# Performance work log

Hardware: AMD Instinct MI355X
Metric: run time of the kernel (lower is better)

Reference implementation:

```python
import jax, jax.numpy as jnp
import numpy as np
import math

B, S, E = 2, 4096, 2048
H, HKV, DK, DV = 16, 4, 128, 128
WIN = 512
EPS = 1e-5
NEG = -1e30


def setup_inputs() -> dict:
    key = jax.random.key(0)
    ks = jax.random.split(key, 8)
    scale = 1.0 / math.sqrt(E)
    return {
        "embeddings": jax.random.normal(ks[0], (B, S, E), dtype=jnp.float32),
        "cos_buffer": jax.random.uniform(ks[1], (2, 1, S, DK), dtype=jnp.float32),
        "sin_buffer": jax.random.uniform(ks[2], (2, 1, S, DK), dtype=jnp.float32),
        "wq": jax.random.normal(ks[3], (E, H * DK), dtype=jnp.float32) * scale,
        "wk": jax.random.normal(ks[4], (E, HKV * DK), dtype=jnp.float32) * scale,
        "wv": jax.random.normal(ks[5], (E, HKV * DV), dtype=jnp.float32) * scale,
        "wo": jax.random.normal(ks[6], (H * DV, E), dtype=jnp.float32) * (1.0 / math.sqrt(H * DV)),
        "window_size": WIN,
    }


def _rotate(f, cos, sin):
    half = f.shape[-1] // 2
    swapped = jnp.concatenate([f[..., half:], f[..., :half]], axis=-1)
    return cos * f + sin * swapped


def reference(embeddings, cos_buffer, sin_buffer, wq, wk, wv, wo, window_size):
    b, s, _ = embeddings.shape
    normed = embeddings * jax.lax.rsqrt(
        jnp.mean(jnp.square(embeddings), axis=-1, keepdims=True) + EPS)
    q = (normed @ wq).reshape(b, s, H, DK).transpose(0, 2, 1, 3)
    k = (normed @ wk).reshape(b, s, HKV, DK).transpose(0, 2, 1, 3)
    v = (normed @ wv).reshape(b, s, HKV, DV).transpose(0, 2, 1, 3)

    q = _rotate(q, cos_buffer[0], sin_buffer[0])
    k = _rotate(k, cos_buffer[1], sin_buffer[1])

    g = H // HKV
    k = jnp.repeat(k, g, axis=1)
    v = jnp.repeat(v, g, axis=1)

    W = window_size
    nb = s // W
    qb = q.reshape(b, H, nb, W, DK)
    kb = k.reshape(b, H, nb, W, DK)
    vb = v.reshape(b, H, nb, W, DV)
    k_prev = jnp.pad(kb, ((0, 0), (0, 0), (1, 0), (0, 0), (0, 0)))[:, :, :nb]
    v_prev = jnp.pad(vb, ((0, 0), (0, 0), (1, 0), (0, 0), (0, 0)))[:, :, :nb]
    kcat = jnp.concatenate([k_prev, kb], axis=3)
    vcat = jnp.concatenate([v_prev, vb], axis=3)

    scores = jnp.einsum('bhnqd,bhnkd->bhnqk', qb, kcat) / math.sqrt(DK)

    i = jnp.arange(W)[:, None]
    j = jnp.arange(2 * W)[None, :]
    base = (j > i) & (j <= i + W)
    blk = jnp.arange(nb)[:, None, None]
    mask = base[None] & ((blk > 0) | (j[None] >= W))
    scores = jnp.where(mask[None, None], scores, NEG)

    probs = jax.nn.softmax(scores, axis=-1)
    out = jnp.einsum('bhnqk,bhnkd->bhnqd', probs, vcat)
    out = out.reshape(b, H, s, DV).transpose(0, 2, 1, 3).reshape(b, s, H * DV)
    out = out @ wo
    return embeddings + out
```

## Files before the change

### kernel.cpp

```cpp
#include <hip/hip_runtime.h>

typedef unsigned short u16;
typedef __attribute__((ext_vector_type(8))) short s16x8;
typedef __attribute__((ext_vector_type(8))) unsigned short u16x8;
typedef __attribute__((ext_vector_type(4))) unsigned short u16x4;
typedef __attribute__((ext_vector_type(4))) float f32x4;

#define DEV __device__ __forceinline__

DEV u16 f2bf(float x) {
  union { float f; unsigned u; } c; c.f = x;
  unsigned r = c.u + 0x7FFFu + ((c.u >> 16) & 1u);
  return (u16)(r >> 16);
}
DEV float bf2f(u16 u) {
  union { unsigned u; float f; } c; c.u = ((unsigned)u) << 16;
  return c.f;
}
DEV void gload_lds16(const void* g, void* l) {
  __builtin_amdgcn_global_load_lds((const __attribute__((address_space(1))) void*)g,
                                   (__attribute__((address_space(3))) void*)l, 16, 0, 0);
}

__global__ __launch_bounds__(256) void k_rmsnorm(const float* __restrict__ emb, u16* __restrict__ X) {
  const int row = blockIdx.x;
  const int t = threadIdx.x;
  const float4* p4 = (const float4*)(emb + (size_t)row * 2048);
  float4 v0 = p4[t * 2], v1 = p4[t * 2 + 1];
  float ss = v0.x * v0.x + v0.y * v0.y + v0.z * v0.z + v0.w * v0.w
           + v1.x * v1.x + v1.y * v1.y + v1.z * v1.z + v1.w * v1.w;
  for (int off = 32; off; off >>= 1) ss += __shfl_xor(ss, off);
  __shared__ float red[4];
  if ((t & 63) == 0) red[t >> 6] = ss;
  __syncthreads();
  float tot = red[0] + red[1] + red[2] + red[3];
  float inv = rsqrtf(tot * (1.0f / 2048.0f) + 1e-5f);
  float v[8] = {v0.x, v0.y, v0.z, v0.w, v1.x, v1.y, v1.z, v1.w};
  u16x8 o;
  for (int j = 0; j < 8; ++j) o[j] = f2bf(v[j] * inv);
  *(u16x8*)(X + (size_t)row * 2048 + t * 8) = o;
}

__global__ __launch_bounds__(256) void k_transpose(const float* __restrict__ src, u16* __restrict__ dst,
                                                   int C, int dstStride) {
  __shared__ float tile[32][33];
  const int bc = blockIdx.x * 32, br = blockIdx.y * 32;
  const int tx = threadIdx.x & 31, ty = threadIdx.x >> 5;
  for (int i = 0; i < 32; i += 8)
    tile[ty + i][tx] = src[(size_t)(br + ty + i) * C + bc + tx];
  __syncthreads();
  for (int i = 0; i < 32; i += 8)
    dst[(size_t)(bc + ty + i) * dstStride + br + tx] = f2bf(tile[tx][ty + i]);
}

template <int EPI>
__global__ __launch_bounds__(256) void k_gemm_bt(const u16* __restrict__ A, const u16* __restrict__ Bt,
                                                 const int N, const int K,
                                                 u16* __restrict__ Cb, const float* __restrict__ Emb,
                                                 float* __restrict__ Cf,
                                                 u16* __restrict__ VtOut, const int vcol0) {
  __shared__ u16 As[128 * 32], Bs[128 * 32];
  const int t = threadIdx.x, w = t >> 6, l = t & 63;
  const int g = l >> 4, cc = l & 15;
  const int wr = w >> 1, wc = w & 1;
  const size_t m0 = (size_t)blockIdx.y * 128, n0 = (size_t)blockIdx.x * 128;
  const int lrow = l >> 2, lcol = (l & 3) * 8;
  f32x4 acc[4][4];
  for (int mi = 0; mi < 4; ++mi)
    for (int ni = 0; ni < 4; ++ni) acc[mi][ni] = (f32x4){0.f, 0.f, 0.f, 0.f};
  for (int k0 = 0; k0 < K; k0 += 32) {
    __syncthreads();
    for (int i = 0; i < 2; ++i) {
      const int ca = w * 2 + i;
      gload_lds16(A + (m0 + ca * 16 + lrow) * K + k0 + lcol, As + ca * 512);
      gload_lds16(Bt + (n0 + ca * 16 + lrow) * K + k0 + lcol, Bs + ca * 512);
    }
    __syncthreads();
    s16x8 a[4], b[4];
    for (int mi = 0; mi < 4; ++mi) a[mi] = *(const s16x8*)&As[(wr * 64 + mi * 16 + cc) * 32 + g * 8];
    for (int ni = 0; ni < 4; ++ni) b[ni] = *(const s16x8*)&Bs[(wc * 64 + ni * 16 + cc) * 32 + g * 8];
    for (int mi = 0; mi < 4; ++mi)
      for (int ni = 0; ni < 4; ++ni)
        acc[mi][ni] = __builtin_amdgcn_mfma_f32_16x16x32_bf16(a[mi], b[ni], acc[mi][ni], 0, 0, 0);
  }
  if (EPI == 1) {
    for (int mi = 0; mi < 4; ++mi)
      for (int ni = 0; ni < 4; ++ni)
        for (int r = 0; r < 4; ++r) {
          const size_t row = m0 + wr * 64 + mi * 16 + g * 4 + r;
          const size_t col = n0 + wc * 64 + ni * 16 + cc;
          Cf[row * N + col] = acc[mi][ni][r] + Emb[row * N + col];
        }
  } else if ((int)n0 >= vcol0) {
    const int hkv = (int)(n0 - vcol0) >> 7;
    const int bb = (int)(m0 >> 12);
    const int s0base = (int)(m0 & 4095);
    u16* vdst = VtOut + (size_t)(bb * 4 + hkv) * 128 * 4096;
    for (int mi = 0; mi < 4; ++mi)
      for (int ni = 0; ni < 4; ++ni) {
        const int d = wc * 64 + ni * 16 + cc;
        const int s = s0base + wr * 64 + mi * 16 + g * 4;
        u16x4 o;
        for (int r = 0; r < 4; ++r) o[r] = f2bf(acc[mi][ni][r]);
        *(u16x4*)(vdst + (size_t)d * 4096 + s) = o;
      }
  } else {
    for (int mi = 0; mi < 4; ++mi)
      for (int ni = 0; ni < 4; ++ni)
        for (int r = 0; r < 4; ++r) {
          const size_t row = m0 + wr * 64 + mi * 16 + g * 4 + r;
          const size_t col = n0 + wc * 64 + ni * 16 + cc;
          Cb[row * N + col] = f2bf(acc[mi][ni][r]);
        }
  }
}

__global__ __launch_bounds__(192) void k_rope(const u16* __restrict__ qkv, const float* __restrict__ cosb,
                                              const float* __restrict__ sinb, u16* __restrict__ Q,
                                              u16* __restrict__ K) {
  const int row = blockIdx.x;
  const int b = row >> 12, s = row & 4095;
  const int t = threadIdx.x;
  const u16* src = qkv + (size_t)row * 3072;
  if (t < 128) {
    const int h = t >> 3, d0 = (t & 7) * 8;
    const float* cp = cosb + (size_t)s * 128;
    const float* sp = sinb + (size_t)s * 128;
    u16x8 lo = *(const u16x8*)(src + h * 128 + d0);
    u16x8 hi = *(const u16x8*)(src + h * 128 + d0 + 64);
    u16x8 olo, ohi;
    for (int j = 0; j < 8; ++j) {
      float fl = bf2f(lo[j]), fh = bf2f(hi[j]);
      olo[j] = f2bf(cp[d0 + j] * fl + sp[d0 + j] * fh);
      ohi[j] = f2bf(cp[d0 + 64 + j] * fh + sp[d0 + 64 + j] * fl);
    }
    u16* dq = Q + (((size_t)b * 16 + h) * 4096 + s) * 128;
    *(u16x8*)(dq + d0) = olo;
    *(u16x8*)(dq + d0 + 64) = ohi;
  } else if (t < 160) {
    const int idx = t - 128, hk = idx >> 3, d0 = (idx & 7) * 8;
    const float* cp = cosb + 524288 + (size_t)s * 128;
    const float* sp = sinb + 524288 + (size_t)s * 128;
    u16x8 lo = *(const u16x8*)(src + 2048 + hk * 128 + d0);
    u16x8 hi = *(const u16x8*)(src + 2048 + hk * 128 + d0 + 64);
    u16x8 olo, ohi;
    for (int j = 0; j < 8; ++j) {
      float fl = bf2f(lo[j]), fh = bf2f(hi[j]);
      olo[j] = f2bf(cp[d0 + j] * fl + sp[d0 + j] * fh);
      ohi[j] = f2bf(cp[d0 + 64 + j] * fh + sp[d0 + 64 + j] * fl);
    }
    u16* dk = K + (((size_t)b * 4 + hk) * 4096 + s) * 128;
    *(u16x8*)(dk + d0) = olo;
    *(u16x8*)(dk + d0 + 64) = ohi;
  }
}

__global__ __launch_bounds__(256) void k_attn(const u16* __restrict__ Q, const u16* __restrict__ K,
                                              const u16* __restrict__ Vt, u16* __restrict__ AO) {
  const int bid = blockIdx.x;
  const int lin = (bid & 7) * 128 + (bid >> 3);
  const int grp = lin >> 7;
  const int b = grp >> 2, hkv = grp & 3;
  const int rem = lin & 127;
  const int h = hkv * 4 + (rem >> 5);
  const int qt = rem & 31;

  const int t = threadIdx.x, w = t >> 6, l = t & 63, g = l >> 4, cc = l & 15;
  const int q0 = qt * 128;
  const u16* Qp = Q + (((size_t)b * 16 + h) * 4096 + q0) * 128;
  const u16* Kp = K + ((size_t)b * 4 + hkv) * 4096 * 128;
  const u16* Vp = Vt + ((size_t)b * 4 + hkv) * 128 * 4096;

  __shared__ u16 Kl[2][32 * 128];
  __shared__ u16 Vl[2][128 * 32];
  __shared__ u16 Ps[4][32 * 40];
  u16* myPs = &Ps[w][0];

  auto stage = [&](int kt, int bufi) {
    for (int pass = 0; pass < 2; ++pass) {
      const int m = pass * 256 + t;
      const int row = m >> 4, cst = m & 15;
      const int cor = cst ^ (row & 7);
      gload_lds16(Kp + (size_t)(kt * 32 + row) * 128 + cor * 8, &Kl[bufi][m * 8]);
    }
    for (int pass = 0; pass < 2; ++pass) {
      const int m = pass * 256 + t;
      const int d = m >> 2, cst = m & 3;
      const int cor = cst ^ (d & 3);
      gload_lds16(Vp + (size_t)d * 4096 + kt * 32 + cor * 8, &Vl[bufi][m * 8]);
    }
  };

  s16x8 qf[2][4];
  for (int mi = 0; mi < 2; ++mi)
    for (int kk = 0; kk < 4; ++kk)
      qf[mi][kk] = *(const s16x8*)(Qp + (size_t)(w * 32 + mi * 16 + cc) * 128 + kk * 32 + g * 8);

  f32x4 accO[2][8];
  for (int mi = 0; mi < 2; ++mi)
    for (int nd = 0; nd < 8; ++nd) accO[mi][nd] = (f32x4){0.f, 0.f, 0.f, 0.f};
  float mrun[2], lrun[2];
  for (int mi = 0; mi < 2; ++mi) { mrun[mi] = -1e30f; lrun[mi] = 0.f; }

  int lo = q0 - 511; if (lo < 0) lo = 0;
  const int kt_lo = lo >> 5, kt_hi = (q0 + 127) >> 5;
  const float scale = 0.08838834764831845f;

  int cur = 0;
  stage(kt_lo, 0);
  __syncthreads();

  for (int kt = kt_lo; kt <= kt_hi; ++kt) {
    if (kt < kt_hi) stage(kt + 1, cur ^ 1);

    f32x4 sc[2][2];
    for (int mi = 0; mi < 2; ++mi)
      for (int nk = 0; nk < 2; ++nk) sc[mi][nk] = (f32x4){0.f, 0.f, 0.f, 0.f};
    __builtin_amdgcn_s_setprio(1);
    for (int kk = 0; kk < 4; ++kk) {
      s16x8 kb[2];
      for (int nk = 0; nk < 2; ++nk) {
        const int row = nk * 16 + cc;
        kb[nk] = *(const s16x8*)&Kl[cur][row * 128 + (((kk * 4 + g) ^ (row & 7)) * 8)];
      }
      for (int mi = 0; mi < 2; ++mi)
        for (int nk = 0; nk < 2; ++nk)
          sc[mi][nk] = __builtin_amdgcn_mfma_f32_16x16x32_bf16(kb[nk], qf[mi][kk], sc[mi][nk], 0, 0, 0);
    }
    __builtin_amdgcn_s_setprio(0);

    const bool full = (kt * 32 >= q0 - 384) && (kt * 32 + 31 <= q0);

    for (int mi = 0; mi < 2; ++mi) {
      const int qpos = q0 + w * 32 + mi * 16 + cc;
      if (full) {
        for (int nk = 0; nk < 2; ++nk)
          for (int r = 0; r < 4; ++r) sc[mi][nk][r] *= scale;
      } else {
        for (int nk = 0; nk < 2; ++nk)
          for (int r = 0; r < 4; ++r) {
            const int kpos = kt * 32 + nk * 16 + g * 4 + r;
            const float v = sc[mi][nk][r] * scale;
            sc[mi][nk][r] = (kpos <= qpos && kpos + 512 > qpos) ? v : -1e30f;
          }
      }
      float rm = sc[mi][0][0];
      for (int nk = 0; nk < 2; ++nk)
        for (int r = 0; r < 4; ++r) rm = fmaxf(rm, sc[mi][nk][r]);
      rm = fmaxf(rm, __shfl_xor(rm, 16));
      rm = fmaxf(rm, __shfl_xor(rm, 32));
      const float mnew = fmaxf(mrun[mi], rm);
      float rs = 0.f;
      if (full) {
        for (int nk = 0; nk < 2; ++nk)
          for (int r = 0; r < 4; ++r) {
            float pv = __expf(sc[mi][nk][r] - mnew);
            sc[mi][nk][r] = pv;
            rs += pv;
          }
      } else {
        for (int nk = 0; nk < 2; ++nk)
          for (int r = 0; r < 4; ++r) {
            float pv = sc[mi][nk][r];
            pv = (pv <= -1e29f) ? 0.f : __expf(pv - mnew);
            sc[mi][nk][r] = pv;
            rs += pv;
          }
      }
      rs += __shfl_xor(rs, 16);
      rs += __shfl_xor(rs, 32);
      const float alpha = __expf(mrun[mi] - mnew);
      mrun[mi] = mnew;
      lrun[mi] = lrun[mi] * alpha + rs;
      for (int nd = 0; nd < 8; ++nd)
        for (int r = 0; r < 4; ++r) accO[mi][nd][r] *= alpha;
      for (int nk = 0; nk < 2; ++nk) {
        u16x4 o;
        for (int r = 0; r < 4; ++r) o[r] = f2bf(sc[mi][nk][r]);
        *(u16x4*)&myPs[(mi * 16 + cc) * 40 + nk * 16 + g * 4] = o;
      }
    }

    __builtin_amdgcn_s_setprio(1);
    {
      s16x8 pa[2];
      for (int mi = 0; mi < 2; ++mi)
        pa[mi] = *(const s16x8*)&myPs[(mi * 16 + cc) * 40 + g * 8];
      for (int nd = 0; nd < 8; ++nd) {
        const int d = nd * 16 + cc;
        s16x8 vb = *(const s16x8*)&Vl[cur][d * 32 + ((g ^ (d & 3)) * 8)];
        for (int mi = 0; mi < 2; ++mi)
          accO[mi][nd] = __builtin_amdgcn_mfma_f32_16x16x32_bf16(vb, pa[mi], accO[mi][nd], 0, 0, 0);
      }
    }
    __builtin_amdgcn_s_setprio(0);

    __syncthreads();
    cur ^= 1;
  }

  u16* op = AO + ((size_t)b * 4096 + q0) * 2048 + (size_t)h * 128;
  for (int mi = 0; mi < 2; ++mi) {
    const float inv = 1.0f / lrun[mi];
    for (int nd = 0; nd < 8; ++nd) {
      u16x4 o;
      for (int r = 0; r < 4; ++r) o[r] = f2bf(accO[mi][nd][r] * inv);
      *(u16x4*)(op + (size_t)(w * 32 + mi * 16 + cc) * 2048 + nd * 16 + g * 4) = o;
    }
  }
}

extern "C" void kernel_launch(void* const* d_in, const int* in_sizes, int n_in,
                              void* d_out, int out_size, void* d_ws, size_t ws_size,
                              hipStream_t stream) {
  const float* emb  = (const float*)d_in[0];
  const float* cosb = (const float*)d_in[1];
  const float* sinb = (const float*)d_in[2];
  const float* wq   = (const float*)d_in[3];
  const float* wk   = (const float*)d_in[4];
  const float* wv   = (const float*)d_in[5];
  const float* wo   = (const float*)d_in[6];
  float* out = (float*)d_out;

  char* ws = (char*)d_ws;
  size_t off = 0;
  auto alloc = [&](size_t bytes) -> void* {
    void* p = ws + off;
    off += (bytes + 255) & ~(size_t)255;
    return p;
  };
  u16* X   = (u16*)alloc((size_t)8192 * 2048 * 2);
  u16* Wt  = (u16*)alloc((size_t)3072 * 2048 * 2);
  u16* Wot = (u16*)alloc((size_t)2048 * 2048 * 2);
  u16* qkv = (u16*)alloc((size_t)8192 * 3072 * 2);
  u16* Qb  = (u16*)alloc((size_t)2 * 16 * 4096 * 128 * 2);
  u16* Kb  = (u16*)alloc((size_t)2 * 4 * 4096 * 128 * 2);
  u16* VtB = (u16*)alloc((size_t)2 * 4 * 128 * 4096 * 2);
  u16* AOb = X;

  k_transpose<<<dim3(64, 64), 256, 0, stream>>>(wq, Wt, 2048, 2048);
  k_transpose<<<dim3(16, 64), 256, 0, stream>>>(wk, Wt + (size_t)2048 * 2048, 512, 2048);
  k_transpose<<<dim3(16, 64), 256, 0, stream>>>(wv, Wt + (size_t)2560 * 2048, 512, 2048);
  k_transpose<<<dim3(64, 64), 256, 0, stream>>>(wo, Wot, 2048, 2048);
  k_rmsnorm<<<8192, 256, 0, stream>>>(emb, X);
  k_gemm_bt<0><<<dim3(24, 64), 256, 0, stream>>>(X, Wt, 3072, 2048, qkv, nullptr, nullptr, VtB, 2560);
  k_rope<<<8192, 192, 0, stream>>>(qkv, cosb, sinb, Qb, Kb);
  k_attn<<<dim3(1024), 256, 0, stream>>>(Qb, Kb, VtB, AOb);
  k_gemm_bt<1><<<dim3(16, 64), 256, 0, stream>>>(AOb, Wot, 2048, 2048, nullptr, emb, out, nullptr, 1 << 30);
}
```

Measured before the change: 408.8 us.

## Replace GEMM with 256x256 double-buffered, swizzled LDS tile kernel

Replaces the 128x128, K=32 single-buffered GEMM with a 256x256, K=64 tile kernel using 8 waves, double-buffered LDS and an XOR swizzle to avoid bank conflicts. The next K tile is prefetched during MFMA work, with setprio around MFMA blocks and an XCD-aware block remap for L2 locality. The aim is higher arithmetic intensity and overlap of global loads with compute in both the QKV and output projections. In exchange it uses far more LDS (128KB) and registers, which limits occupancy, and the grid shrinks to 384 and 256 blocks.

Result: faster. 355.8 us (-13.0%).

```diff
diff --git a/kernel.cpp b/kernel.cpp
--- a/kernel.cpp
+++ b/kernel.cpp
@@ -54,62 +54,126 @@
 }
 
 template <int EPI>
-__global__ __launch_bounds__(256) void k_gemm_bt(const u16* __restrict__ A, const u16* __restrict__ Bt,
-                                                 const int N, const int K,
+__global__ __launch_bounds__(512) void k_gemm256(const u16* __restrict__ A, const u16* __restrict__ Bt,
+                                                 const int N, const int K, const int NBN,
                                                  u16* __restrict__ Cb, const float* __restrict__ Emb,
                                                  float* __restrict__ Cf,
                                                  u16* __restrict__ VtOut, const int vcol0) {
-  __shared__ u16 As[128 * 32], Bs[128 * 32];
-  const int t = threadIdx.x, w = t >> 6, l = t & 63;
-  const int g = l >> 4, cc = l & 15;
-  const int wr = w >> 1, wc = w & 1;
-  const size_t m0 = (size_t)blockIdx.y * 128, n0 = (size_t)blockIdx.x * 128;
-  const int lrow = l >> 2, lcol = (l & 3) * 8;
-  f32x4 acc[4][4];
-  for (int mi = 0; mi < 4; ++mi)
+  __shared__ u16 Asm[2][256 * 64];
+  __shared__ u16 Bsm[2][256 * 64];
+  const int t = threadIdx.x, w = t >> 6, l = t & 63, g = (l >> 4), cc = l & 15;
+  const int wm = w >> 2, wn = w & 3;
+
+  const int cpx = gridDim.x >> 3;
+  const int lin = (blockIdx.x & 7) * cpx + (blockIdx.x >> 3);
+  const int bm = lin / NBN, bn = lin % NBN;
+  const size_t m0 = (size_t)bm * 256, n0 = (size_t)bn * 256;
+
+  const int srow = t >> 3, sch = t & 7;
+
+  auto stA = [&](int kt, int p, int pass) {
+    const int row = pass * 64 + srow;
+    const int c2 = sch ^ (row & 7);
+    gload_lds16(A + (m0 + row) * K + kt * 64 + c2 * 8, &Asm[p][row * 64 + sch * 8]);
+  };
+  auto stB = [&](int kt, int p, int pass) {
+    const int row = pass * 64 + srow;
+    const int c2 = sch ^ (row & 7);
+    gload_lds16(Bt + (n0 + row) * K + kt * 64 + c2 * 8, &Bsm[p][row * 64 + sch * 8]);
+  };
+
+  f32x4 acc[8][4];
+#pragma unroll
+  for (int mi = 0; mi < 8; ++mi)
+#pragma unroll
     for (int ni = 0; ni < 4; ++ni) acc[mi][ni] = (f32x4){0.f, 0.f, 0.f, 0.f};
-  for (int k0 = 0; k0 < K; k0 += 32) {
+
+  const int NT = K >> 6;
+#pragma unroll
+  for (int pass = 0; pass < 4; ++pass) { stA(0, 0, pass); stB(0, 0, pass); }
+  __syncthreads();
+
+  for (int kt = 0; kt < NT; ++kt) {
+    const int p = kt & 1;
+    const bool pf = (kt + 1 < NT);
+    const u16* Ap = &Asm[p][0];
+    const u16* Bp = &Bsm[p][0];
+
+    s16x8 bf[2][4];
+#pragma unroll
+    for (int kk = 0; kk < 2; ++kk)
+#pragma unroll
+      for (int ni = 0; ni < 4; ++ni) {
+        const int row = wn * 64 + ni * 16 + cc;
+        bf[kk][ni] = *(const s16x8*)&Bp[row * 64 + (((kk * 4 + g) ^ (row & 7)) * 8)];
+      }
+
+#pragma unroll
+    for (int q = 0; q < 4; ++q) {
+      s16x8 af[2][2];
+#pragma unroll
+      for (int kk = 0; kk < 2; ++kk)
+#pragma unroll
+        for (int m2 = 0; m2 < 2; ++m2) {
+          const int row = wm * 128 + (q * 2 + m2) * 16 + cc;
+          af[kk][m2] = *(const s16x8*)&Ap[row * 64 + (((kk * 4 + g) ^ (row & 7)) * 8)];
+        }
+      if (pf) {
+        if (q == 0) { stA(kt + 1, p ^ 1, 0); stA(kt + 1, p ^ 1, 1); }
+        else if (q == 1) { stA(kt + 1, p ^ 1, 2); stA(kt + 1, p ^ 1, 3); }
+        else if (q == 2) { stB(kt + 1, p ^ 1, 0); stB(kt + 1, p ^ 1, 1); }
+        else { stB(kt + 1, p ^ 1, 2); stB(kt + 1, p ^ 1, 3); }
+      }
+      __builtin_amdgcn_s_barrier();
+      __builtin_amdgcn_s_setprio(1);
+#pragma unroll
+      for (int m2 = 0; m2 < 2; ++m2)
+#pragma unroll
+        for (int ni = 0; ni < 4; ++ni)
+#pragma unroll
+          for (int kk = 0; kk < 2; ++kk)
+            acc[q * 2 + m2][ni] =
+                __builtin_amdgcn_mfma_f32_16x16x32_bf16(af[kk][m2], bf[kk][ni], acc[q * 2 + m2][ni], 0, 0, 0);
+      __builtin_amdgcn_s_setprio(0);
+    }
     __syncthreads();
-    for (int i = 0; i < 2; ++i) {
-      const int ca = w * 2 + i;
-      gload_lds16(A + (m0 + ca * 16 + lrow) * K + k0 + lcol, As + ca * 512);
-      gload_lds16(Bt + (n0 + ca * 16 + lrow) * K + k0 + lcol, Bs + ca * 512);
-    }
-    __syncthreads();
-    s16x8 a[4], b[4];
-    for (int mi = 0; mi < 4; ++mi) a[mi] = *(const s16x8*)&As[(wr * 64 + mi * 16 + cc) * 32 + g * 8];
-    for (int ni = 0; ni < 4; ++ni) b[ni] = *(const s16x8*)&Bs[(wc * 64 + ni * 16 + cc) * 32 + g * 8];
-    for (int mi = 0; mi < 4; ++mi)
+  }
+
+  if (EPI == 1) {
+#pragma unroll
+    for (int mi = 0; mi < 8; ++mi)
+#pragma unroll
       for (int ni = 0; ni < 4; ++ni)
-        acc[mi][ni] = __builtin_amdgcn_mfma_f32_16x16x32_bf16(a[mi], b[ni], acc[mi][ni], 0, 0, 0);
-  }
-  if (EPI == 1) {
-    for (int mi = 0; mi < 4; ++mi)
-      for (int ni = 0; ni < 4; ++ni)
+#pragma unroll
         for (int r = 0; r < 4; ++r) {
-          const size_t row = m0 + wr * 64 + mi * 16 + g * 4 + r;
-          const size_t col = n0 + wc * 64 + ni * 16 + cc;
+          const size_t row = m0 + wm * 128 + mi * 16 + g * 4 + r;
+          const size_t col = n0 + wn * 64 + ni * 16 + cc;
           Cf[row * N + col] = acc[mi][ni][r] + Emb[row * N + col];
         }
   } else if ((int)n0 >= vcol0) {
-    const int hkv = (int)(n0 - vcol0) >> 7;
     const int bb = (int)(m0 >> 12);
     const int s0base = (int)(m0 & 4095);
-    u16* vdst = VtOut + (size_t)(bb * 4 + hkv) * 128 * 4096;
-    for (int mi = 0; mi < 4; ++mi)
+#pragma unroll
+    for (int mi = 0; mi < 8; ++mi)
+#pragma unroll
       for (int ni = 0; ni < 4; ++ni) {
-        const int d = wc * 64 + ni * 16 + cc;
-        const int s = s0base + wr * 64 + mi * 16 + g * 4;
+        const int dcol = (int)(n0 - vcol0) + wn * 64 + ni * 16 + cc;
+        const int hkv = dcol >> 7, d = dcol & 127;
+        const int s = s0base + wm * 128 + mi * 16 + g * 4;
         u16x4 o;
+#pragma unroll
         for (int r = 0; r < 4; ++r) o[r] = f2bf(acc[mi][ni][r]);
-        *(u16x4*)(vdst + (size_t)d * 4096 + s) = o;
+        *(u16x4*)(VtOut + ((size_t)(bb * 4 + hkv) * 128 + d) * 4096 + s) = o;
       }
   } else {
-    for (int mi = 0; mi < 4; ++mi)
+#pragma unroll
+    for (int mi = 0; mi < 8; ++mi)
+#pragma unroll
       for (int ni = 0; ni < 4; ++ni)
+#pragma unroll
         for (int r = 0; r < 4; ++r) {
-          const size_t row = m0 + wr * 64 + mi * 16 + g * 4 + r;
-          const size_t col = n0 + wc * 64 + ni * 16 + cc;
+          const size_t row = m0 + wm * 128 + mi * 16 + g * 4 + r;
+          const size_t col = n0 + wn * 64 + ni * 16 + cc;
           Cb[row * N + col] = f2bf(acc[mi][ni][r]);
         }
   }
@@ -343,8 +407,8 @@
   k_transpose<<<dim3(16, 64), 256, 0, stream>>>(wv, Wt + (size_t)2560 * 2048, 512, 2048);
   k_transpose<<<dim3(64, 64), 256, 0, stream>>>(wo, Wot, 2048, 2048);
   k_rmsnorm<<<8192, 256, 0, stream>>>(emb, X);
-  k_gemm_bt<0><<<dim3(24, 64), 256, 0, stream>>>(X, Wt, 3072, 2048, qkv, nullptr, nullptr, VtB, 2560);
+  k_gemm256<0><<<dim3(384), 512, 0, stream>>>(X, Wt, 3072, 2048, 12, qkv, nullptr, nullptr, VtB, 2560);
   k_rope<<<8192, 192, 0, stream>>>(qkv, cosb, sinb, Qb, Kb);
   k_attn<<<dim3(1024), 256, 0, stream>>>(Qb, Kb, VtB, AOb);
-  k_gemm_bt<1><<<dim3(16, 64), 256, 0, stream>>>(AOb, Wot, 2048, 2048, nullptr, emb, out, nullptr, 1 << 30);
-}
+  k_gemm256<1><<<dim3(256), 512, 0, stream>>>(AOb, Wot, 2048, 2048, 8, nullptr, emb, out, nullptr, 1 << 30);
+}
```
